# Kernel optimization log

Measured on AMD Instinct MI355X. Metric: run time of the kernel, lower is better.

## Reference

```python
import jax, jax.numpy as jnp
import numpy as np

B, S, D, H, DFF = 2, 2048, 1024, 16, 4096
DK = D // H
EPS = 1e-05


def setup_inputs() -> dict:
    key = jax.random.key(0)
    ks = jax.random.split(key, 10)
    s = 0.02
    return {
        "x": jax.random.normal(ks[0], (B, S, D), jnp.float32),
        "src_mask": jnp.ones((B, 1, 1, S), jnp.int32),
        "wq": jax.random.normal(ks[1], (D, D), jnp.float32) * s,
        "wk": jax.random.normal(ks[2], (D, D), jnp.float32) * s,
        "wv": jax.random.normal(ks[3], (D, D), jnp.float32) * s,
        "wo": jax.random.normal(ks[4], (D, D), jnp.float32) * s,
        "w1": jax.random.normal(ks[5], (D, DFF), jnp.float32) * s,
        "b1": jnp.zeros((DFF,), jnp.float32),
        "w2": jax.random.normal(ks[6], (DFF, D), jnp.float32) * s,
        "b2": jnp.zeros((D,), jnp.float32),
        "gamma1": jnp.ones((), jnp.float32),
        "beta1": jnp.ones((), jnp.float32),
        "gamma2": jnp.ones((), jnp.float32),
        "beta2": jnp.ones((), jnp.float32),
    }


def layer_norm(x, gamma, beta):
    # torch.var uses unbiased estimator (ddof=1); gamma/beta are scalars
    mean = jnp.mean(x, axis=-1, keepdims=True)
    var = jnp.var(x, axis=-1, keepdims=True, ddof=1)
    return (x - mean) * gamma / jnp.sqrt(var + EPS) + beta


def mha(x, wq, wk, wv, wo):
    # Note: source's masked_fill is non-in-place with discarded result -> mask has no effect.
    q = (x @ wq).reshape(B, S, H, DK).transpose(0, 2, 1, 3)
    k = (x @ wk).reshape(B, S, H, DK).transpose(0, 2, 1, 3)
    v = (x @ wv).reshape(B, S, H, DK).transpose(0, 2, 1, 3)
    scores = jnp.einsum('bhqd,bhkd->bhqk', q, k) / jnp.sqrt(jnp.float32(DK))
    attn = jax.nn.softmax(scores, axis=-1)
    out = jnp.einsum('bhqk,bhkd->bhqd', attn, v)
    out = out.transpose(0, 2, 1, 3).reshape(B, S, D)
    return out @ wo


def reference(x, src_mask, wq, wk, wv, wo, w1, b1, w2, b2,
              gamma1, beta1, gamma2, beta2):
    # residual 1: attention (dropout = identity in eval)
    x = layer_norm(x + mha(x, wq, wk, wv, wo), gamma1, beta1)
    # residual 2: FFN
    ff = jax.nn.relu(x @ w1 + b1) @ w2 + b2
    x = layer_norm(x + ff, gamma2, beta2)
    return x
```

## Files before the change

kernel.cpp:

```cpp
#include <hip/hip_runtime.h>
#include <cstdio>

constexpr int B_   = 2;
constexpr int S_   = 2048;
constexpr int D_   = 1024;
constexpr int H_   = 16;
constexpr int DFF_ = 4096;
constexpr int DK_  = D_ / H_;
constexpr int M_   = B_ * S_;
constexpr float EPS_ = 1e-5f;
constexpr size_t MEGE = 1u << 20;
constexpr size_t QKV_STRIDE = 4 * MEGE;
constexpr float QSCALE_ = 0.18033688011112042f;

typedef __attribute__((ext_vector_type(8))) short bf16x8;
typedef __attribute__((ext_vector_type(4))) float f32x4;

__device__ __forceinline__ float bf2f(unsigned int u) {
    return __uint_as_float(u << 16);
}
__device__ __forceinline__ unsigned short f2bf(float f) {
    unsigned int u = __float_as_uint(f);
    unsigned int r = u + 0x7fffu + ((u >> 16) & 1u);
    return (unsigned short)(r >> 16);
}
__device__ __forceinline__ unsigned short f2bf_rz(float f) {
    return (unsigned short)(__float_as_uint(f) >> 16);
}
__device__ __forceinline__ float exp2_fast(float x) {
    float r;
    asm("v_exp_f32 %0, %1" : "=v"(r) : "v"(x));
    return r;
}

__device__ __forceinline__ void gload_lds16(const unsigned short* g, unsigned short* l) {
    __builtin_amdgcn_global_load_lds(
        (const __attribute__((address_space(1))) unsigned int*)g,
        (__attribute__((address_space(3))) unsigned int*)l, 16, 0, 0);
}

__device__ __forceinline__ void tr32(const float* __restrict__ W, unsigned short* __restrict__ Wt,
                                     int K, int N, int bx, int by, float* t )
{
    const int tx = threadIdx.x & 31, ty = threadIdx.x >> 5;
    const int n0 = bx * 32, k0 = by * 32;
    #pragma unroll
    for (int p = 0; p < 4; ++p)
        t[(ty + p * 8) * 33 + tx] = W[(size_t)(k0 + ty + p * 8) * N + n0 + tx];
    __syncthreads();
    #pragma unroll
    for (int p = 0; p < 4; ++p)
        Wt[(size_t)(n0 + ty + p * 8) * K + k0 + tx] = f2bf(t[tx * 33 + ty + p * 8]);
}

__global__ __launch_bounds__(256)
void prep_k(const float* __restrict__ wq, const float* __restrict__ wk,
            const float* __restrict__ wv, const float* __restrict__ wo,
            const float* __restrict__ w1, const float* __restrict__ w2,
            const float* __restrict__ x,
            unsigned short* __restrict__ wqt, unsigned short* __restrict__ wkt,
            unsigned short* __restrict__ wvt, unsigned short* __restrict__ wot,
            unsigned short* __restrict__ w1t, unsigned short* __restrict__ w2t,
            unsigned short* __restrict__ xb)
{
    __shared__ float t[32 * 33];
    const int bid = blockIdx.x;
    if (bid < 4096) {
        const int z = bid >> 10, rem = bid & 1023;
        const float* W = (z == 0) ? wq : (z == 1) ? wk : (z == 2) ? wv : wo;
        unsigned short* Wt = (z == 0) ? wqt : (z == 1) ? wkt : (z == 2) ? wvt : wot;
        tr32(W, Wt, D_, D_, rem & 31, rem >> 5, t);
    } else if (bid < 8192) {
        const int rem = bid - 4096;
        tr32(w1, w1t, D_, DFF_, rem & 127, rem >> 7, t);
    } else if (bid < 12288) {
        const int rem = bid - 8192;
        tr32(w2, w2t, DFF_, D_, rem & 31, rem >> 5, t);
    } else {
        const int i = (bid - 12288) * 256 + threadIdx.x;
        float4 f = reinterpret_cast<const float4*>(x)[i];
        ushort4 u;
        u.x = f2bf(f.x); u.y = f2bf(f.y); u.z = f2bf(f.z); u.w = f2bf(f.w);
        reinterpret_cast<ushort4*>(xb)[i] = u;
    }
}

template<int BM, int OMODE, bool RELU>
__global__ __launch_bounds__(512, 2)
void mg2_k(const unsigned short* __restrict__ A,
           const unsigned short* __restrict__ Bt,
           const float* __restrict__ bias,
           unsigned short* __restrict__ C,
           int M, int N, int K, int Kld)
{
    constexpr int MI  = BM / 64;
    constexpr int AMH = (BM == 128) ? 2 : 1;
    __shared__ __align__(16) unsigned short As[2][BM * 64];
    __shared__ __align__(16) unsigned short Bs[2][256 * 64];

    const int z = blockIdx.z;
    A  += (size_t)z * K;
    Bt += (size_t)z * K;
    C  += (size_t)z * ((size_t)M * N);

    const int tid  = threadIdx.x;
    const int w    = tid >> 6, lane = tid & 63;
    const int l15  = lane & 15, quad = lane >> 4;
    const int wm   = w >> 2, wn = w & 3;
    const int m0   = blockIdx.y * BM, n0 = blockIdx.x * 256;
    const int NT   = K >> 6;

    const int srow = lane >> 3;
    const int schk = (lane & 7) ^ srow;
    const int rsw  = l15 & 7;

    f32x4 acc[2][MI][2][2];
    #pragma unroll
    for (int mh = 0; mh < 2; ++mh)
        #pragma unroll
        for (int mi = 0; mi < MI; ++mi)
            #pragma unroll
            for (int nh = 0; nh < 2; ++nh)
                #pragma unroll
                for (int nj = 0; nj < 2; ++nj)
                    acc[mh][mi][nh][nj] = (f32x4){0.f, 0.f, 0.f, 0.f};

    bf16x8 aA[AMH][MI][2];
    bf16x8 b0[2][2], b1[2][2];

    auto stage = [&](int tile, int type) {
        if (tile >= NT) return;
        const int buf = tile & 1;
        unsigned short* dst; const unsigned short* src; int r0;
        if (BM == 256) {
            if      (type == 0) { dst = &As[buf][0];        src = A;  r0 = m0; }
            else if (type == 1) { dst = &Bs[buf][0];        src = Bt; r0 = n0; }
            else if (type == 2) { dst = &Bs[buf][128 * 64]; src = Bt; r0 = n0 + 128; }
            else                { dst = &As[buf][128 * 64]; src = A;  r0 = m0 + 128; }
        } else {
            if      (type == 0) { dst = &Bs[buf][0];        src = Bt; r0 = n0; }
            else if (type == 1) { dst = &As[buf][0];        src = A;  r0 = m0; }
            else                { dst = &Bs[buf][128 * 64]; src = Bt; r0 = n0 + 128; }
        }
        const int k0 = tile * 64;
        #pragma unroll
        for (int g = 0; g < 2; ++g) {
            const int r = w * 16 + g * 8 + srow;
            gload_lds16(src + (size_t)(r0 + r) * Kld + k0 + schk * 8,
                        dst + (w * 16 + g * 8) * 64);
        }
    };
    auto rdA = [&](int buf, int mh, int amh) {
        const unsigned short* base = &As[buf][(BM == 256 && mh) ? 128 * 64 : 0];
        #pragma unroll
        for (int mi = 0; mi < MI; ++mi) {
            const int row = (BM == 256) ? (wm * 64 + mi * 16 + l15)
                                        : (wm * 64 + mh * 32 + mi * 16 + l15);
            const unsigned short* rp = base + row * 64;
            aA[amh][mi][0] = *reinterpret_cast<const bf16x8*>(rp + ((quad    ) ^ rsw) * 8);
            aA[amh][mi][1] = *reinterpret_cast<const bf16x8*>(rp + ((quad + 4) ^ rsw) * 8);
        }
    };
    auto rdB = [&](int buf, int nh, bf16x8 (&b)[2][2]) {
        const unsigned short* base = &Bs[buf][nh ? 128 * 64 : 0];
        #pragma unroll
        for (int nj = 0; nj < 2; ++nj) {
            const int row = wn * 32 + nj * 16 + l15;
            const unsigned short* rp = base + row * 64;
            b[nj][0] = *reinterpret_cast<const bf16x8*>(rp + ((quad    ) ^ rsw) * 8);
            b[nj][1] = *reinterpret_cast<const bf16x8*>(rp + ((quad + 4) ^ rsw) * 8);
        }
    };
    auto mm = [&](int mh, int amh, int nh, bf16x8 (&b)[2][2]) {
        __builtin_amdgcn_s_setprio(1);
        #pragma unroll
        for (int mi = 0; mi < MI; ++mi)
            #pragma unroll
            for (int nj = 0; nj < 2; ++nj) {
                acc[mh][mi][nh][nj] = __builtin_amdgcn_mfma_f32_16x16x32_bf16(
                    aA[amh][mi][0], b[nj][0], acc[mh][mi][nh][nj], 0, 0, 0);
                acc[mh][mi][nh][nj] = __builtin_amdgcn_mfma_f32_16x16x32_bf16(
                    aA[amh][mi][1], b[nj][1], acc[mh][mi][nh][nj], 0, 0, 0);
            }
        __builtin_amdgcn_s_setprio(0);
    };

    if (BM == 256) {
        stage(0, 0); stage(0, 1); stage(0, 2); stage(0, 3);
        stage(1, 0); stage(1, 1); stage(1, 2);
    } else {
        stage(0, 0); stage(0, 1); stage(0, 2);
        stage(1, 0); stage(1, 1);
    }

    for (int t = 0; t < NT; ++t) {
        const int cur = t & 1;
        if (t == NT - 1)    asm volatile("s_waitcnt vmcnt(0)" ::: "memory");
        else if (BM == 256) asm volatile("s_waitcnt vmcnt(6)" ::: "memory");
        else                asm volatile("s_waitcnt vmcnt(4)" ::: "memory");
        __builtin_amdgcn_s_barrier();

        if (BM == 256) {
            rdA(cur, 0, 0); rdB(cur, 0, b0); stage(t + 1, 3);
            __builtin_amdgcn_s_barrier();
            asm volatile("s_waitcnt lgkmcnt(0)" ::: "memory");
            mm(0, 0, 0, b0);
            __builtin_amdgcn_s_barrier();
            rdB(cur, 1, b1); stage(t + 2, 0);
            __builtin_amdgcn_s_barrier();
            asm volatile("s_waitcnt lgkmcnt(0)" ::: "memory");
            mm(0, 0, 1, b1);
            __builtin_amdgcn_s_barrier();
            rdA(cur, 1, 0); stage(t + 2, 1);
            __builtin_amdgcn_s_barrier();
            asm volatile("s_waitcnt lgkmcnt(0)" ::: "memory");
            mm(1, 0, 0, b0);
            __builtin_amdgcn_s_barrier();
            stage(t + 2, 2);
            __builtin_amdgcn_s_barrier();
            asm volatile("s_waitcnt lgkmcnt(0)" ::: "memory");
            mm(1, 0, 1, b1);
        } else {
            rdA(cur, 0, 0); rdA(cur, 1, 1); rdB(cur, 0, b0); stage(t + 1, 2);
            __builtin_amdgcn_s_barrier();
            asm volatile("s_waitcnt lgkmcnt(0)" ::: "memory");
            mm(0, 0, 0, b0); mm(1, 1, 0, b0);
            __builtin_amdgcn_s_barrier();
            rdB(cur, 1, b1); stage(t + 2, 0); stage(t + 2, 1);
            __builtin_amdgcn_s_barrier();
            asm volatile("s_waitcnt lgkmcnt(0)" ::: "memory");
            mm(0, 0, 1, b1); mm(1, 1, 1, b1);
        }
    }

    #pragma unroll
    for (int mh = 0; mh < 2; ++mh)
        #pragma unroll
        for (int mi = 0; mi < MI; ++mi) {
            const int mrow = (BM == 256) ? (mh * 128 + wm * 64 + mi * 16)
                                         : (wm * 64 + mh * 32 + mi * 16);
            #pragma unroll
            for (int r = 0; r < 4; ++r) {
                const int m = m0 + mrow + quad * 4 + r;
                #pragma unroll
                for (int nh = 0; nh < 2; ++nh)
                    #pragma unroll
                    for (int nj = 0; nj < 2; ++nj) {
                        const int n = n0 + nh * 128 + wn * 32 + nj * 16 + l15;
                        float v = acc[mh][mi][nh][nj][r];
                        if (bias) v += bias[n];
                        if (RELU) v = fmaxf(v, 0.0f);
                        size_t o;
                        if (OMODE == 2) {
                            int mat = n >> 10, nn = n & 1023;
                            int b = m >> 11, s = m & 2047;
                            int h = nn >> 6, dk = nn & 63;
                            if (mat == 0) v *= QSCALE_;
                            o = (size_t)mat * QKV_STRIDE + (((size_t)b * H_ + h) * S_ + s) * DK_ + dk;
                        } else {
                            o = (size_t)m * N + n;
                        }
                        C[o] = f2bf(v);
                    }
            }
        }
}

__device__ __forceinline__ float wave_sum(float v) {
    #pragma unroll
    for (int off = 32; off > 0; off >>= 1) v += __shfl_down(v, off, 64);
    return v;
}

constexpr int TQ_ = 128;
constexpr int TK_ = 64;
constexpr int NT_ = S_ / TK_;

__global__ __launch_bounds__(512)
void fattn_k(const unsigned short* __restrict__ Qm, const unsigned short* __restrict__ Km,
             const unsigned short* __restrict__ Vm, unsigned short* __restrict__ O)
{
    const int bh  = blockIdx.x >> 4;
    const int qt  = blockIdx.x & 15;
    const int tid = threadIdx.x;
    const int w = tid >> 6, lane = tid & 63;
    const int quad = lane >> 4, l15 = lane & 15;
    const int sw = l15 & 7;

    __shared__ __align__(16) unsigned short Ks[2][TK_][64];
    __shared__ __align__(16) unsigned short Vt[2][80][64];
    __shared__ __align__(16) unsigned short Ps[8][16][64];

    bf16x8 qf0, qf1;
    {
        const unsigned short* qp = Qm + ((size_t)bh * S_ + qt * TQ_ + w * 16 + l15) * DK_;
        qf0 = *reinterpret_cast<const bf16x8*>(qp + quad * 8);
        qf1 = *reinterpret_cast<const bf16x8*>(qp + 32 + quad * 8);
    }

    f32x4 o[4];
    f32x4 o4;
    #pragma unroll
    for (int n = 0; n < 4; ++n) o[n] = (f32x4){0.f, 0.f, 0.f, 0.f};
    o4 = (f32x4){0.f, 0.f, 0.f, 0.f};

    const unsigned short* kg0 = Km + (size_t)bh * S_ * DK_;
    const unsigned short* vg0 = Vm + (size_t)bh * S_ * DK_;
    const int dgrp = tid >> 4;
    const int vkp  = tid & 15;
    const int srow = lane >> 3;
    const int schk = (lane & 7) ^ srow;

    auto stageK = [&](int t, int buf) {
        const unsigned short* src = kg0 + (size_t)t * TK_ * DK_;
        const int wk = w - 4;
        #pragma unroll
        for (int g = 0; g < 2; ++g) {
            const int r0 = wk * 16 + g * 8;
            gload_lds16(src + (size_t)(r0 + srow) * DK_ + schk * 8, &Ks[buf][r0][0]);
        }
    };
    auto loadV = [&](int t, ushort4 (&vp)[4]) {
        const unsigned short* vg = vg0 + (size_t)t * TK_ * DK_;
        #pragma unroll
        for (int p = 0; p < 4; ++p)
            vp[p] = reinterpret_cast<const ushort4*>(vg + (size_t)(vkp + p * 16) * DK_)[dgrp];
    };
    auto storeVt = [&](int buf, ushort4 (&vp)[4]) {
        char* base = reinterpret_cast<char*>(&Vt[buf][dgrp * 4][0]);
        const int cs = vkp >> 1, ch = (vkp & 1) << 3;
        ushort4 pk;
        pk.x = vp[0].x; pk.y = vp[1].x; pk.z = vp[2].x; pk.w = vp[3].x;
        *reinterpret_cast<ushort4*>(base + 0 * 128 + (((cs ^ ((dgrp * 4 + 0) & 7)) << 4) + ch)) = pk;
        pk.x = vp[0].y; pk.y = vp[1].y; pk.z = vp[2].y; pk.w = vp[3].y;
        *reinterpret_cast<ushort4*>(base + 1 * 128 + (((cs ^ ((dgrp * 4 + 1) & 7)) << 4) + ch)) = pk;
        pk.x = vp[0].z; pk.y = vp[1].z; pk.z = vp[2].z; pk.w = vp[3].z;
        *reinterpret_cast<ushort4*>(base + 2 * 128 + (((cs ^ ((dgrp * 4 + 2) & 7)) << 4) + ch)) = pk;
        pk.x = vp[0].w; pk.y = vp[1].w; pk.z = vp[2].w; pk.w = vp[3].w;
        *reinterpret_cast<ushort4*>(base + 3 * 128 + (((cs ^ ((dgrp * 4 + 3) & 7)) << 4) + ch)) = pk;
    };

    if (w >= 4) stageK(0, 0);
    else {
        ushort4 vp0[4];
        loadV(0, vp0);
        storeVt(0, vp0);
    }
    for (int idx = tid; idx < 2 * 16 * 64; idx += 512) {
        const int b  = idx >> 10;
        const int rr = (idx >> 6) & 15;
        const int cc = idx & 63;
        Vt[b][64 + rr][((cc >> 3) ^ (rr & 7)) * 8 + (cc & 7)] =
            (rr == 0) ? (unsigned short)0x3F80 : (unsigned short)0;
    }

    for (int t = 0; t < NT_; ++t) {
        const int cur = t & 1, nxt = cur ^ 1;
        __syncthreads();

        const bool hn = (t + 1 < NT_);
        ushort4 vp[4];
        if (hn) { if (w >= 4) stageK(t + 1, nxt); else loadV(t + 1, vp); }

        f32x4 s[4];
        __builtin_amdgcn_s_setprio(1);
        #pragma unroll
        for (int n = 0; n < 4; ++n) {
            const unsigned short* kp = &Ks[cur][n * 16 + l15][0];
            bf16x8 b0 = *reinterpret_cast<const bf16x8*>(kp + ((quad ^ sw) << 3));
            bf16x8 b1 = *reinterpret_cast<const bf16x8*>(kp + (((quad + 4) ^ sw) << 3));
            f32x4 a2 = (f32x4){0.f, 0.f, 0.f, 0.f};
            a2 = __builtin_amdgcn_mfma_f32_16x16x32_bf16(qf0, b0, a2, 0, 0, 0);
            a2 = __builtin_amdgcn_mfma_f32_16x16x32_bf16(qf1, b1, a2, 0, 0, 0);
            s[n] = a2;
        }
        __builtin_amdgcn_s_setprio(0);

        #pragma unroll
        for (int r = 0; r < 4; ++r) {
            ushort4 pk;
            pk.x = f2bf_rz(exp2_fast(s[0][r]));
            pk.y = f2bf_rz(exp2_fast(s[1][r]));
            pk.z = f2bf_rz(exp2_fast(s[2][r]));
            pk.w = f2bf_rz(exp2_fast(s[3][r]));
            const int R = quad * 4 + r;
            *reinterpret_cast<ushort4*>(
                reinterpret_cast<char*>(&Ps[w][R][0]) +
                ((((l15 >> 1) ^ (R & 7)) << 4) + ((l15 & 1) << 3))) = pk;
        }

        if (hn && w < 4) storeVt(nxt, vp);

        bf16x8 pa0, pa1;
        {
            const unsigned short* pp = &Ps[w][l15][0];
            pa0 = *reinterpret_cast<const bf16x8*>(pp + ((quad ^ sw) << 3));
            pa1 = *reinterpret_cast<const bf16x8*>(pp + (((quad + 4) ^ sw) << 3));
        }
        __builtin_amdgcn_s_setprio(1);
        #pragma unroll
        for (int n = 0; n < 4; ++n) {
            const unsigned short* vb = &Vt[cur][n * 16 + l15][0];
            bf16x8 vb0 = *reinterpret_cast<const bf16x8*>(vb + ((quad ^ sw) << 3));
            bf16x8 vb1 = *reinterpret_cast<const bf16x8*>(vb + (((quad + 4) ^ sw) << 3));
            o[n] = __builtin_amdgcn_mfma_f32_16x16x32_bf16(pa0, vb0, o[n], 0, 0, 0);
            o[n] = __builtin_amdgcn_mfma_f32_16x16x32_bf16(pa1, vb1, o[n], 0, 0, 0);
        }
        {
            const unsigned short* vb = &Vt[cur][64 + l15][0];
            bf16x8 vb40 = *reinterpret_cast<const bf16x8*>(vb + ((quad ^ sw) << 3));
            bf16x8 vb41 = *reinterpret_cast<const bf16x8*>(vb + (((quad + 4) ^ sw) << 3));
            o4 = __builtin_amdgcn_mfma_f32_16x16x32_bf16(pa0, vb40, o4, 0, 0, 0);
            o4 = __builtin_amdgcn_mfma_f32_16x16x32_bf16(pa1, vb41, o4, 0, 0, 0);
        }
        __builtin_amdgcn_s_setprio(0);
    }

    const int b = bh >> 4, h = bh & 15;
    #pragma unroll
    for (int r = 0; r < 4; ++r) {
        float lrv = __shfl(o4[r], lane & 0x30, 64);
        float inv = 1.0f / lrv;
        int q = qt * TQ_ + w * 16 + quad * 4 + r;
        unsigned short* op = O + ((size_t)b * S_ + q) * D_ + h * DK_;
        #pragma unroll
        for (int n = 0; n < 4; ++n)
            op[n * 16 + l15] = f2bf(o[n][r] * inv);
    }
}

template<bool HAS_BIAS, bool RES_F32, bool OUT_F32>
__global__ __launch_bounds__(256)
void lnr_k(const unsigned short* __restrict__ P0, const unsigned short* __restrict__ P1,
           const void* __restrict__ res, const float* __restrict__ bias,
           const float* __restrict__ gp, const float* __restrict__ bp,
           void* __restrict__ Out)
{
    const int row = blockIdx.x;
    const int tid = threadIdx.x;
    const int lane = tid & 63, wave = tid >> 6;
    __shared__ float rs[4], rss[4];

    const size_t i4 = (size_t)row * 256 + tid;
    const ushort4 a = reinterpret_cast<const ushort4*>(P0)[i4];
    const ushort4 b = reinterpret_cast<const ushort4*>(P1)[i4];
    float v0 = bf2f(a.x) + bf2f(b.x);
    float v1 = bf2f(a.y) + bf2f(b.y);
    float v2 = bf2f(a.z) + bf2f(b.z);
    float v3 = bf2f(a.w) + bf2f(b.w);
    if (RES_F32) {
        float4 rv = reinterpret_cast<const float4*>(res)[i4];
        v0 += rv.x; v1 += rv.y; v2 += rv.z; v3 += rv.w;
    } else {
        ushort4 rv = reinterpret_cast<const ushort4*>(res)[i4];
        v0 += bf2f(rv.x); v1 += bf2f(rv.y); v2 += bf2f(rv.z); v3 += bf2f(rv.w);
    }
    if (HAS_BIAS) {
        float4 bv = reinterpret_cast<const float4*>(bias)[tid];
        v0 += bv.x; v1 += bv.y; v2 += bv.z; v3 += bv.w;
    }

    float s  = v0 + v1 + v2 + v3;
    float ss = v0*v0 + v1*v1 + v2*v2 + v3*v3;
    s = wave_sum(s);
    ss = wave_sum(ss);
    if (lane == 0) { rs[wave] = s; rss[wave] = ss; }
    __syncthreads();
    const float stot  = rs[0] + rs[1] + rs[2] + rs[3];
    const float sstot = rss[0] + rss[1] + rss[2] + rss[3];
    const float mean = stot / (float)D_;
    const float var  = (sstot - (float)D_ * mean * mean) / (float)(D_ - 1);
    const float scl = gp[0] * rsqrtf(var + EPS_);
    const float be = bp[0];

    float o0 = (v0 - mean) * scl + be;
    float o1 = (v1 - mean) * scl + be;
    float o2 = (v2 - mean) * scl + be;
    float o3 = (v3 - mean) * scl + be;
    if (OUT_F32) {
        reinterpret_cast<float4*>(Out)[i4] = make_float4(o0, o1, o2, o3);
    } else {
        ushort4 o;
        o.x = f2bf(o0); o.y = f2bf(o1); o.z = f2bf(o2); o.w = f2bf(o3);
        reinterpret_cast<ushort4*>(Out)[i4] = o;
    }
}

extern "C" void kernel_launch(void* const* d_in, const int* in_sizes, int n_in,
                              void* d_out, int out_size, void* d_ws, size_t ws_size,
                              hipStream_t stream)
{
    const float* x   = (const float*)d_in[0];
    const float* wq  = (const float*)d_in[2];
    const float* wk  = (const float*)d_in[3];
    const float* wv  = (const float*)d_in[4];
    const float* wo  = (const float*)d_in[5];
    const float* w1  = (const float*)d_in[6];
    const float* b1  = (const float*)d_in[7];
    const float* w2  = (const float*)d_in[8];
    const float* b2  = (const float*)d_in[9];
    const float* g1  = (const float*)d_in[10];
    const float* be1 = (const float*)d_in[11];
    const float* g2  = (const float*)d_in[12];
    const float* be2 = (const float*)d_in[13];

    unsigned short* ws = (unsigned short*)d_ws;
    const size_t need_bytes = 32 * MEGE * 2;
    if (ws_size < need_bytes) {
        fprintf(stderr, "kernel_launch: ws too small (%zu < %zu)\n", ws_size, need_bytes);
    }
    unsigned short* wqt = ws + 0 * MEGE;
    unsigned short* wkt = ws + 1 * MEGE;
    unsigned short* wvt = ws + 2 * MEGE;
    unsigned short* wot = ws + 3 * MEGE;
    unsigned short* w1t = ws + 4 * MEGE;
    unsigned short* w2t = ws + 8 * MEGE;
    unsigned short* xb  = ws + 12 * MEGE;
    unsigned short* Q   = ws + 16 * MEGE;
    unsigned short* K   = ws + 20 * MEGE;
    unsigned short* V   = ws + 24 * MEGE;
    unsigned short* AO  = ws + 28 * MEGE;
    unsigned short* x1  = xb;
    unsigned short* WP  = ws + 16 * MEGE;
    unsigned short* h1  = ws + 16 * MEGE;
    unsigned short* FP  = ws + 0 * MEGE;

    prep_k<<<dim3(16384), 256, 0, stream>>>(wq, wk, wv, wo, w1, w2, x,
                                            wqt, wkt, wvt, wot, w1t, w2t, xb);

    mg2_k<256, 2, false><<<dim3(3 * D_ / 256, M_ / 256), 512, 0, stream>>>(
        xb, wqt, nullptr, Q, M_, 3 * D_, D_, D_);

    fattn_k<<<dim3(B_ * H_ * (S_ / TQ_)), 512, 0, stream>>>(Q, K, V, AO);

    mg2_k<128, 0, false><<<dim3(D_ / 256, M_ / 128, 2), 512, 0, stream>>>(
        AO, wot, nullptr, WP, M_, D_, D_ / 2, D_);

    lnr_k<false, true, false><<<dim3(M_), 256, 0, stream>>>(
        WP, WP + 4 * MEGE, x, nullptr, g1, be1, x1);

    mg2_k<256, 0, true><<<dim3(DFF_ / 256, M_ / 256), 512, 0, stream>>>(
        x1, w1t, b1, h1, M_, DFF_, D_, D_);

    mg2_k<128, 0, false><<<dim3(D_ / 256, M_ / 128, 2), 512, 0, stream>>>(
        h1, w2t, nullptr, FP, M_, D_, DFF_ / 2, DFF_);

    lnr_k<true, false, true><<<dim3(M_), 256, 0, stream>>>(
        FP, FP + 4 * MEGE, x1, b2, g2, be2, d_out);
}
```

Measured before the change: 325.7 us.

## Add 1024-thread 256x256 GEMM kernel for QKV and FFN1 projections

Adds a new GEMM kernel that uses 16 waves (1024 threads) per 256x256 tile. Each wave computes a 64x64 sub-tile using a double-buffered LDS pipeline with swizzled loads and raised wave priority around the MFMA block. The kernel replaces the 512-thread mg2_k for the QKV projection and the first FFN matmul. The aim is more latency hiding per tile and less register pressure per wave, at the cost of a single block per CU and extra barriers per k-step.

```diff
diff --git a/kernel.cpp b/kernel.cpp
--- a/kernel.cpp
+++ b/kernel.cpp
@@ -85,6 +85,116 @@
     }
 }
 
+template<int OMODE, bool RELU>
+__global__ __launch_bounds__(1024, 1)
+void mg3_k(const unsigned short* __restrict__ A,
+           const unsigned short* __restrict__ Bt,
+           const float* __restrict__ bias,
+           unsigned short* __restrict__ C,
+           int M, int N, int K, int Kld)
+{
+    __shared__ __align__(16) unsigned short As[2][256 * 64];
+    __shared__ __align__(16) unsigned short Bs[2][256 * 64];
+
+    const int tid = threadIdx.x;
+    const int w = tid >> 6, lane = tid & 63;
+    const int l15 = lane & 15, quad = lane >> 4;
+    const int wm = w >> 2, wn = w & 3;
+    const int m0 = blockIdx.y * 256, n0 = blockIdx.x * 256;
+    const int NT = K >> 6;
+
+    const int srow = lane >> 3;
+    const int schk = (lane & 7) ^ srow;
+    const int rsw  = l15 & 7;
+
+    f32x4 acc[4][4];
+    #pragma unroll
+    for (int i = 0; i < 4; ++i)
+        #pragma unroll
+        for (int j = 0; j < 4; ++j) acc[i][j] = (f32x4){0.f, 0.f, 0.f, 0.f};
+
+    auto stageAB = [&](int tile) {
+        if (tile >= NT) return;
+        const int buf = tile & 1;
+        const int k0 = tile * 64;
+        #pragma unroll
+        for (int g = 0; g < 2; ++g) {
+            const int r = w * 16 + g * 8;
+            gload_lds16(A + (size_t)(m0 + r + srow) * Kld + k0 + schk * 8, &As[buf][r * 64]);
+        }
+        #pragma unroll
+        for (int g = 0; g < 2; ++g) {
+            const int r = w * 16 + g * 8;
+            gload_lds16(Bt + (size_t)(n0 + r + srow) * Kld + k0 + schk * 8, &Bs[buf][r * 64]);
+        }
+    };
+
+    bf16x8 a[4], b[4];
+    auto rd = [&](int buf, int h) {
+        #pragma unroll
+        for (int i = 0; i < 4; ++i) {
+            const unsigned short* rp = &As[buf][(wm * 64 + i * 16 + l15) * 64];
+            a[i] = *reinterpret_cast<const bf16x8*>(rp + (((quad + 4 * h) ^ rsw) << 3));
+        }
+        #pragma unroll
+        for (int j = 0; j < 4; ++j) {
+            const unsigned short* rp = &Bs[buf][(wn * 64 + j * 16 + l15) * 64];
+            b[j] = *reinterpret_cast<const bf16x8*>(rp + (((quad + 4 * h) ^ rsw) << 3));
+        }
+    };
+    auto mm16 = [&]() {
+        __builtin_amdgcn_s_setprio(1);
+        #pragma unroll
+        for (int i = 0; i < 4; ++i)
+            #pragma unroll
+            for (int j = 0; j < 4; ++j)
+                acc[i][j] = __builtin_amdgcn_mfma_f32_16x16x32_bf16(a[i], b[j], acc[i][j], 0, 0, 0);
+        __builtin_amdgcn_s_setprio(0);
+    };
+
+    stageAB(0);
+
+    for (int t = 0; t < NT; ++t) {
+        const int cur = t & 1;
+        asm volatile("s_waitcnt vmcnt(0)" ::: "memory");
+        __builtin_amdgcn_s_barrier();
+        stageAB(t + 1);
+        rd(cur, 0);
+        __builtin_amdgcn_s_barrier();
+        asm volatile("s_waitcnt lgkmcnt(0)" ::: "memory");
+        mm16();
+        rd(cur, 1);
+        __builtin_amdgcn_s_barrier();
+        asm volatile("s_waitcnt lgkmcnt(0)" ::: "memory");
+        mm16();
+    }
+
+    #pragma unroll
+    for (int i = 0; i < 4; ++i)
+        #pragma unroll
+        for (int r = 0; r < 4; ++r) {
+            const int m = m0 + wm * 64 + i * 16 + quad * 4 + r;
+            #pragma unroll
+            for (int j = 0; j < 4; ++j) {
+                const int n = n0 + wn * 64 + j * 16 + l15;
+                float v = acc[i][j][r];
+                if (bias) v += bias[n];
+                if (RELU) v = fmaxf(v, 0.0f);
+                size_t o;
+                if (OMODE == 2) {
+                    int mat = n >> 10, nn = n & 1023;
+                    int bb = m >> 11, s = m & 2047;
+                    int h = nn >> 6, dk = nn & 63;
+                    if (mat == 0) v *= QSCALE_;
+                    o = (size_t)mat * QKV_STRIDE + (((size_t)bb * H_ + h) * S_ + s) * DK_ + dk;
+                } else {
+                    o = (size_t)m * N + n;
+                }
+                C[o] = f2bf(v);
+            }
+        }
+}
+
 template<int BM, int OMODE, bool RELU>
 __global__ __launch_bounds__(512, 2)
 void mg2_k(const unsigned short* __restrict__ A,
@@ -528,7 +638,7 @@
     prep_k<<<dim3(16384), 256, 0, stream>>>(wq, wk, wv, wo, w1, w2, x,
                                             wqt, wkt, wvt, wot, w1t, w2t, xb);
 
-    mg2_k<256, 2, false><<<dim3(3 * D_ / 256, M_ / 256), 512, 0, stream>>>(
+    mg3_k<2, false><<<dim3(3 * D_ / 256, M_ / 256), 1024, 0, stream>>>(
         xb, wqt, nullptr, Q, M_, 3 * D_, D_, D_);
 
     fattn_k<<<dim3(B_ * H_ * (S_ / TQ_)), 512, 0, stream>>>(Q, K, V, AO);
@@ -539,7 +649,7 @@
     lnr_k<false, true, false><<<dim3(M_), 256, 0, stream>>>(
         WP, WP + 4 * MEGE, x, nullptr, g1, be1, x1);
 
-    mg2_k<256, 0, true><<<dim3(DFF_ / 256, M_ / 256), 512, 0, stream>>>(
+    mg3_k<0, true><<<dim3(DFF_ / 256, M_ / 256), 1024, 0, stream>>>(
         x1, w1t, b1, h1, M_, DFF_, D_, D_);
 
     mg2_k<128, 0, false><<<dim3(D_ / 256, M_ / 128, 2), 512, 0, stream>>>(
```

New measurement: 324.7 us. About the same (-0.3%).
